# Kernel optimization log

Measured on AMD Instinct MI355X. Metric: run time of the kernel, lower is better.

## Reference

```python
import jax, jax.numpy as jnp
import numpy as np

N, IN_F, OUT_F = 4096, 512, 256
GRAPH_DENSITY = 0.01
NEG_FILL = -1e11  # torch code uses -100000000000.0


def _normalise(g, remove_diagonal):
    # dense branch of normalise_graph (self_connection=False)
    if remove_diagonal:
        g = g - jnp.diag(jnp.diag(g))
    s = g.sum(axis=1)
    s = jnp.where(s == 0.0, 1.0, s)
    d = s ** -0.5
    return d[:, None] * g * d[None, :]


def setup_inputs() -> dict:
    key = jax.random.key(0)
    k1, k2, k3, k4, k5 = jax.random.split(key, 5)
    x = jax.random.normal(k1, (N, IN_F), jnp.float32)
    graph = (jax.random.uniform(k2, (N, N)) < GRAPH_DENSITY).astype(jnp.float32)
    # fc/weight: kaiming-normal-like init
    weight = jax.random.normal(k3, (OUT_F, IN_F), jnp.float32) * np.float32(np.sqrt(2.0 / IN_F))
    t_s = jax.random.normal(k4, (1, OUT_F), jnp.float32) * 0.05
    t_r = jax.random.normal(k5, (1, OUT_F), jnp.float32) * 0.05
    return {"x": x, "graph": graph, "weight": weight, "t_s": t_s, "t_r": t_r}


def reference(x, graph, weight, t_s, t_r):
    # H_ = input @ weight.T   (no bias, no dropout)
    H = x @ weight.T  # [N, OUT_F]

    # get_mask(graph, power=1): normalise(remove_diag) then normalise again
    mask = _normalise(_normalise(graph, remove_diagonal=True), remove_diagonal=False)  # [N, N]

    # get_edge_index_attention, dense path, attention_features == 1
    C1 = jax.nn.leaky_relu(H @ t_s.T, negative_slope=0.2)       # [N, 1]
    C2 = jax.nn.leaky_relu(H @ t_r.T, negative_slope=0.2).T    # [1, N]
    S = (mask * C1 + mask * C2) * 0.5                           # [N, N]
    S = jnp.where(mask <= 0.0, NEG_FILL, S)
    A = jax.nn.softmax(S, axis=1)                               # neighbourhood softmax

    # normalise_graph(A, remove_diagonal=False, self_connection=True), dense path
    A = A + jnp.eye(A.shape[0], dtype=A.dtype)
    s = A.sum(axis=1)
    s = jnp.where(s == 0.0, 1.0, s)
    d = s ** -0.5
    C = d[:, None] * A * d[None, :]

    return C @ H  # [N, OUT_F]
```

## Files before the change

### kernel.cpp

```cpp
#include <hip/hip_runtime.h>
#include <hip/hip_bf16.h>
#include <math.h>

#define N 4096
#define IN_F 512
#define OUT_F 256
#define CAP 128

typedef __attribute__((ext_vector_type(8))) short short8;
typedef __attribute__((ext_vector_type(4))) float float4v;

static __device__ __forceinline__ ushort f2bf(float f) {
  unsigned u = __float_as_uint(f);
  unsigned rnd = 0x7fffu + ((u >> 16) & 1u);
  return (ushort)((u + rnd) >> 16);
}

__global__ __launch_bounds__(256) void build_csr(
    const float* __restrict__ g, int* __restrict__ cols,
    int* __restrict__ deg, float* __restrict__ d1,
    float* __restrict__ c1r, float* __restrict__ c2r) {
  int i = blockIdx.x;
  __shared__ int s_cnt;
  if (threadIdx.x == 0) { s_cnt = 0; c1r[i] = 0.f; c2r[i] = 0.f; }
  __syncthreads();
  const float4* row4 = (const float4*)(g + (size_t)i * N);
  int lane = threadIdx.x & 63;
  for (int it = threadIdx.x; it < N / 4; it += 256) {
    float4 v = row4[it];
    int jb = it * 4;
    bool nz0 = (v.x != 0.f) && (jb + 0 != i);
    bool nz1 = (v.y != 0.f) && (jb + 1 != i);
    bool nz2 = (v.z != 0.f) && (jb + 2 != i);
    bool nz3 = (v.w != 0.f) && (jb + 3 != i);
    unsigned long long m0 = __ballot(nz0);
    unsigned long long m1 = __ballot(nz1);
    unsigned long long m2 = __ballot(nz2);
    unsigned long long m3 = __ballot(nz3);
    int p0 = __popcll(m0), p1 = __popcll(m1), p2 = __popcll(m2), p3 = __popcll(m3);
    int total = p0 + p1 + p2 + p3;
    if (total > 0) {
      int base;
      if (lane == 0) base = atomicAdd(&s_cnt, total);
      base = __shfl(base, 0);
      unsigned long long ltm = (1ull << lane) - 1ull;
      if (nz0) { int p = base + __popcll(m0 & ltm);                 if (p < CAP) cols[(size_t)i * CAP + p] = jb + 0; }
      if (nz1) { int p = base + p0 + __popcll(m1 & ltm);            if (p < CAP) cols[(size_t)i * CAP + p] = jb + 1; }
      if (nz2) { int p = base + p0 + p1 + __popcll(m2 & ltm);       if (p < CAP) cols[(size_t)i * CAP + p] = jb + 2; }
      if (nz3) { int p = base + p0 + p1 + p2 + __popcll(m3 & ltm);  if (p < CAP) cols[(size_t)i * CAP + p] = jb + 3; }
    }
  }
  __syncthreads();
  if (threadIdx.x == 0) {
    int c = s_cnt;
    deg[i] = (c > CAP) ? CAP : c;
    d1[i] = (c == 0) ? 1.f : rsqrtf((float)c);
  }
}

#define LDST 72
__global__ __launch_bounds__(256) void gemm_fused(
    const float* __restrict__ x, const float* __restrict__ wgt,
    const float* __restrict__ ts, const float* __restrict__ tr,
    const int* __restrict__ cols, const int* __restrict__ deg,
    const float* __restrict__ d1, float* __restrict__ w,
    float* __restrict__ H, float* __restrict__ c1r, float* __restrict__ c2r) {
  int bid = blockIdx.x;
  if (bid >= 256) {
    int i = (bid - 256) * 256 + threadIdx.x;
    int dgi = deg[i];
    float sum = 0.f;
    for (int k = 0; k < dgi; ++k) sum += d1[cols[(size_t)i * CAP + k]];
    float s2 = d1[i] * sum;
    float dd2 = (s2 == 0.f) ? 1.f : rsqrtf(s2);
    w[i] = d1[i] * dd2;
    return;
  }
  __shared__ __align__(16) ushort As[64 * LDST];
  __shared__ __align__(16) ushort Bs[64 * LDST];
  int bm = (bid >> 2) * 64;
  int bn = (bid & 3) * 64;
  int tid = threadIdx.x;
  int lane = tid & 63;
  int wv = tid >> 6;
  int wm = (wv >> 1) * 32, wn = (wv & 1) * 32;

  float4v acc[2][2] = {{{0.f,0.f,0.f,0.f},{0.f,0.f,0.f,0.f}},
                       {{0.f,0.f,0.f,0.f},{0.f,0.f,0.f,0.f}}};

  for (int k0 = 0; k0 < IN_F; k0 += 64) {
    #pragma unroll
    for (int p = 0; p < 4; ++p) {
      int idx = p * 256 + tid;
      int row = idx >> 4;
      int cg = idx & 15;
      float4 va = *(const float4*)(x   + (size_t)(bm + row) * IN_F + k0 + cg * 4);
      float4 vb = *(const float4*)(wgt + (size_t)(bn + row) * IN_F + k0 + cg * 4);
      ushort4 pa, pb;
      pa.x = f2bf(va.x); pa.y = f2bf(va.y); pa.z = f2bf(va.z); pa.w = f2bf(va.w);
      pb.x = f2bf(vb.x); pb.y = f2bf(vb.y); pb.z = f2bf(vb.z); pb.w = f2bf(vb.w);
      *(ushort4*)(As + row * LDST + cg * 4) = pa;
      *(ushort4*)(Bs + row * LDST + cg * 4) = pb;
    }
    __syncthreads();
    #pragma unroll
    for (int kk = 0; kk < 64; kk += 32) {
      int kof = kk + (lane >> 4) * 8;
      short8 a0 = *(const short8*)(As + (wm +      (lane & 15)) * LDST + kof);
      short8 a1 = *(const short8*)(As + (wm + 16 + (lane & 15)) * LDST + kof);
      short8 b0 = *(const short8*)(Bs + (wn +      (lane & 15)) * LDST + kof);
      short8 b1 = *(const short8*)(Bs + (wn + 16 + (lane & 15)) * LDST + kof);
      acc[0][0] = __builtin_amdgcn_mfma_f32_16x16x32_bf16(a0, b0, acc[0][0], 0, 0, 0);
      acc[0][1] = __builtin_amdgcn_mfma_f32_16x16x32_bf16(a0, b1, acc[0][1], 0, 0, 0);
      acc[1][0] = __builtin_amdgcn_mfma_f32_16x16x32_bf16(a1, b0, acc[1][0], 0, 0, 0);
      acc[1][1] = __builtin_amdgcn_mfma_f32_16x16x32_bf16(a1, b1, acc[1][1], 0, 0, 0);
    }
    __syncthreads();
  }
  int ccol = lane & 15;
  int crow = (lane >> 4) * 4;
  float ts0 = ts[bn + wn + ccol],      ts1 = ts[bn + wn + 16 + ccol];
  float tr0 = tr[bn + wn + ccol],      tr1 = tr[bn + wn + 16 + ccol];
  #pragma unroll
  for (int rt = 0; rt < 2; ++rt) {
    #pragma unroll
    for (int r = 0; r < 4; ++r) {
      float ps = acc[rt][0][r] * ts0 + acc[rt][1][r] * ts1;
      float pr = acc[rt][0][r] * tr0 + acc[rt][1][r] * tr1;
      #pragma unroll
      for (int off = 1; off < 16; off <<= 1) {
        ps += __shfl_xor(ps, off);
        pr += __shfl_xor(pr, off);
      }
      if (ccol == 0) {
        int row = bm + wm + rt * 16 + crow + r;
        atomicAdd(&c1r[row], ps);
        atomicAdd(&c2r[row], pr);
      }
    }
  }
  #pragma unroll
  for (int rt = 0; rt < 2; ++rt)
    #pragma unroll
    for (int ct = 0; ct < 2; ++ct)
      #pragma unroll
      for (int r = 0; r < 4; ++r) {
        int gr = bm + wm + rt * 16 + crow + r;
        int gc = bn + wn + ct * 16 + ccol;
        H[(size_t)gr * OUT_F + gc] = acc[rt][ct][r];
      }
}

__global__ __launch_bounds__(256) void aggregate(
    const float* __restrict__ H, const int* __restrict__ cols,
    const int* __restrict__ deg, const float* __restrict__ w,
    const float* __restrict__ c1r, const float* __restrict__ c2r,
    float* __restrict__ out) {
  __shared__ int sJ[4][CAP];
  __shared__ float sA[4][CAP];
  int wv = threadIdx.x >> 6;
  int lane = threadIdx.x & 63;
  int i = blockIdx.x * 4 + wv;
  int dgi = deg[i];
  float wi = w[i];
  float c1v = c1r[i];
  float ci = c1v > 0.f ? c1v : 0.2f * c1v;

  float S0 = -1e30f, S1 = -1e30f;
  int j0 = 0, j1 = 0;
  if (lane < dgi) {
    j0 = cols[(size_t)i * CAP + lane];
    float c2v = c2r[j0];
    float cj = c2v > 0.f ? c2v : 0.2f * c2v;
    S0 = 0.5f * wi * w[j0] * (ci + cj);
  }
  if (lane + 64 < dgi) {
    j1 = cols[(size_t)i * CAP + lane + 64];
    float c2v = c2r[j1];
    float cj = c2v > 0.f ? c2v : 0.2f * c2v;
    S1 = 0.5f * wi * w[j1] * (ci + cj);
  }
  float mx = fmaxf(S0, S1);
  #pragma unroll
  for (int off = 32; off > 0; off >>= 1) mx = fmaxf(mx, __shfl_xor(mx, off));
  float e0 = (lane < dgi) ? __expf(S0 - mx) : 0.f;
  float e1 = (lane + 64 < dgi) ? __expf(S1 - mx) : 0.f;
  float Z = e0 + e1;
  #pragma unroll
  for (int off = 32; off > 0; off >>= 1) Z += __shfl_xor(Z, off);
  if (lane < dgi)      { sJ[wv][lane] = j0;        sA[wv][lane] = e0 / Z; }
  if (lane + 64 < dgi) { sJ[wv][lane + 64] = j1;   sA[wv][lane + 64] = e1 / Z; }
  __syncthreads();

  float4 accv = ((const float4*)(H + (size_t)i * OUT_F))[lane];
  if (dgi > 0) {
    int k = 0;
    for (; k + 1 < dgi; k += 2) {
      int ja = sJ[wv][k], jb = sJ[wv][k + 1];
      float aa = sA[wv][k], ab = sA[wv][k + 1];
      float4 ha = ((const float4*)(H + (size_t)ja * OUT_F))[lane];
      float4 hb = ((const float4*)(H + (size_t)jb * OUT_F))[lane];
      accv.x += aa * ha.x + ab * hb.x;
      accv.y += aa * ha.y + ab * hb.y;
      accv.z += aa * ha.z + ab * hb.z;
      accv.w += aa * ha.w + ab * hb.w;
    }
    if (k < dgi) {
      int ja = sJ[wv][k];
      float aa = sA[wv][k];
      float4 ha = ((const float4*)(H + (size_t)ja * OUT_F))[lane];
      accv.x += aa * ha.x; accv.y += aa * ha.y;
      accv.z += aa * ha.z; accv.w += aa * ha.w;
    }
  } else {
    float4 s = {0.f, 0.f, 0.f, 0.f};
    for (int r = 0; r < N; ++r) {
      float4 h = ((const float4*)(H + (size_t)r * OUT_F))[lane];
      s.x += h.x; s.y += h.y; s.z += h.z; s.w += h.w;
    }
    const float inv = 1.f / (float)N;
    accv.x += s.x * inv; accv.y += s.y * inv;
    accv.z += s.z * inv; accv.w += s.w * inv;
  }
  float4 o;
  o.x = 0.5f * accv.x; o.y = 0.5f * accv.y;
  o.z = 0.5f * accv.z; o.w = 0.5f * accv.w;
  ((float4*)(out + (size_t)i * OUT_F))[lane] = o;
}

extern "C" void kernel_launch(void* const* d_in, const int* in_sizes, int n_in,
                              void* d_out, int out_size, void* d_ws, size_t ws_size,
                              hipStream_t stream) {
  const float* x     = (const float*)d_in[0];
  const float* graph = (const float*)d_in[1];
  const float* wgt   = (const float*)d_in[2];
  const float* ts    = (const float*)d_in[3];
  const float* tr    = (const float*)d_in[4];
  float* out = (float*)d_out;

  char* ws = (char*)d_ws;
  float* H    = (float*)(ws);
  int*   cols = (int*)  (ws + (size_t)4 * 1024 * 1024);
  int*   deg  = (int*)  (ws + (size_t)6 * 1024 * 1024);
  float* d1   = (float*)(ws + (size_t)6 * 1024 * 1024 + 16384);
  float* w    = (float*)(ws + (size_t)6 * 1024 * 1024 + 32768);
  float* c1r  = (float*)(ws + (size_t)6 * 1024 * 1024 + 49152);
  float* c2r  = (float*)(ws + (size_t)6 * 1024 * 1024 + 65536);

  build_csr<<<N, 256, 0, stream>>>(graph, cols, deg, d1, c1r, c2r);
  gemm_fused<<<272, 256, 0, stream>>>(x, wgt, ts, tr, cols, deg, d1, w, H, c1r, c2r);
  aggregate<<<N / 4, 256, 0, stream>>>(H, cols, deg, w, c1r, c2r, out);
}
```

Baseline: 137.8 us.

## Co-schedule CSR build with GEMM and move row stats into separate kernel

Merges the CSR-building kernel into the GEMM launch as extra blocks, so the dense graph scan and the bf16 MFMA projection run concurrently instead of back to back. The c1/c2 atomics are removed from the GEMM epilogue. A new rowstats kernel computes the attention projections from H, the degree normalisation, and packed per-row coefficients (ab, uv), which lets aggregate compute each score with two FMAs. The aggregation loop is unrolled by four for more memory-level parallelism. The cost is an extra launch and a re-read of H.

```diff
diff --git a/kernel.cpp b/kernel.cpp
--- a/kernel.cpp
+++ b/kernel.cpp
@@ -1,11 +1,11 @@
 #include <hip/hip_runtime.h>
-#include <hip/hip_bf16.h>
 #include <math.h>
 
 #define N 4096
 #define IN_F 512
 #define OUT_F 256
 #define CAP 128
+#define LDST 72
 
 typedef __attribute__((ext_vector_type(8))) short short8;
 typedef __attribute__((ext_vector_type(4))) float float4v;
@@ -16,72 +16,62 @@
   return (ushort)((u + rnd) >> 16);
 }
 
-__global__ __launch_bounds__(256) void build_csr(
-    const float* __restrict__ g, int* __restrict__ cols,
-    int* __restrict__ deg, float* __restrict__ d1,
-    float* __restrict__ c1r, float* __restrict__ c2r) {
-  int i = blockIdx.x;
-  __shared__ int s_cnt;
-  if (threadIdx.x == 0) { s_cnt = 0; c1r[i] = 0.f; c2r[i] = 0.f; }
-  __syncthreads();
-  const float4* row4 = (const float4*)(g + (size_t)i * N);
-  int lane = threadIdx.x & 63;
-  for (int it = threadIdx.x; it < N / 4; it += 256) {
-    float4 v = row4[it];
-    int jb = it * 4;
-    bool nz0 = (v.x != 0.f) && (jb + 0 != i);
-    bool nz1 = (v.y != 0.f) && (jb + 1 != i);
-    bool nz2 = (v.z != 0.f) && (jb + 2 != i);
-    bool nz3 = (v.w != 0.f) && (jb + 3 != i);
-    unsigned long long m0 = __ballot(nz0);
-    unsigned long long m1 = __ballot(nz1);
-    unsigned long long m2 = __ballot(nz2);
-    unsigned long long m3 = __ballot(nz3);
-    int p0 = __popcll(m0), p1 = __popcll(m1), p2 = __popcll(m2), p3 = __popcll(m3);
-    int total = p0 + p1 + p2 + p3;
-    if (total > 0) {
-      int base;
-      if (lane == 0) base = atomicAdd(&s_cnt, total);
-      base = __shfl(base, 0);
-      unsigned long long ltm = (1ull << lane) - 1ull;
-      if (nz0) { int p = base + __popcll(m0 & ltm);                 if (p < CAP) cols[(size_t)i * CAP + p] = jb + 0; }
-      if (nz1) { int p = base + p0 + __popcll(m1 & ltm);            if (p < CAP) cols[(size_t)i * CAP + p] = jb + 1; }
-      if (nz2) { int p = base + p0 + p1 + __popcll(m2 & ltm);       if (p < CAP) cols[(size_t)i * CAP + p] = jb + 2; }
-      if (nz3) { int p = base + p0 + p1 + p2 + __popcll(m3 & ltm);  if (p < CAP) cols[(size_t)i * CAP + p] = jb + 3; }
-    }
-  }
-  __syncthreads();
-  if (threadIdx.x == 0) {
-    int c = s_cnt;
-    deg[i] = (c > CAP) ? CAP : c;
-    d1[i] = (c == 0) ? 1.f : rsqrtf((float)c);
-  }
-}
-
-#define LDST 72
-__global__ __launch_bounds__(256) void gemm_fused(
-    const float* __restrict__ x, const float* __restrict__ wgt,
-    const float* __restrict__ ts, const float* __restrict__ tr,
-    const int* __restrict__ cols, const int* __restrict__ deg,
-    const float* __restrict__ d1, float* __restrict__ w,
-    float* __restrict__ H, float* __restrict__ c1r, float* __restrict__ c2r) {
-  int bid = blockIdx.x;
-  if (bid >= 256) {
-    int i = (bid - 256) * 256 + threadIdx.x;
-    int dgi = deg[i];
-    float sum = 0.f;
-    for (int k = 0; k < dgi; ++k) sum += d1[cols[(size_t)i * CAP + k]];
-    float s2 = d1[i] * sum;
-    float dd2 = (s2 == 0.f) ? 1.f : rsqrtf(s2);
-    w[i] = d1[i] * dd2;
-    return;
-  }
+static __device__ __forceinline__ float leaky(float v) {
+  return v > 0.f ? v : 0.2f * v;
+}
+
+__global__ __launch_bounds__(256) void csr_gemm(
+    const float* __restrict__ g, const float* __restrict__ x,
+    const float* __restrict__ wgt,
+    int* __restrict__ cols, int* __restrict__ deg, float* __restrict__ d1,
+    float* __restrict__ H) {
   __shared__ __align__(16) ushort As[64 * LDST];
   __shared__ __align__(16) ushort Bs[64 * LDST];
+  __shared__ int s_cnt;
+  int bid = blockIdx.x;
+  int tid = threadIdx.x;
+  int lane = tid & 63;
+
+  if (bid >= 256) {
+    int i = bid - 256;
+    if (tid == 0) s_cnt = 0;
+    __syncthreads();
+    const float4* row4 = (const float4*)(g + (size_t)i * N);
+    for (int it = tid; it < N / 4; it += 256) {
+      float4 v = row4[it];
+      int jb = it * 4;
+      bool nz0 = (v.x != 0.f) && (jb + 0 != i);
+      bool nz1 = (v.y != 0.f) && (jb + 1 != i);
+      bool nz2 = (v.z != 0.f) && (jb + 2 != i);
+      bool nz3 = (v.w != 0.f) && (jb + 3 != i);
+      unsigned long long m0 = __ballot(nz0);
+      unsigned long long m1 = __ballot(nz1);
+      unsigned long long m2 = __ballot(nz2);
+      unsigned long long m3 = __ballot(nz3);
+      int p0 = __popcll(m0), p1 = __popcll(m1), p2 = __popcll(m2), p3 = __popcll(m3);
+      int total = p0 + p1 + p2 + p3;
+      if (total > 0) {
+        int base;
+        if (lane == 0) base = atomicAdd(&s_cnt, total);
+        base = __shfl(base, 0);
+        unsigned long long ltm = (1ull << lane) - 1ull;
+        if (nz0) { int p = base + __popcll(m0 & ltm);                 if (p < CAP) cols[(size_t)i * CAP + p] = jb + 0; }
+        if (nz1) { int p = base + p0 + __popcll(m1 & ltm);            if (p < CAP) cols[(size_t)i * CAP + p] = jb + 1; }
+        if (nz2) { int p = base + p0 + p1 + __popcll(m2 & ltm);       if (p < CAP) cols[(size_t)i * CAP + p] = jb + 2; }
+        if (nz3) { int p = base + p0 + p1 + p2 + __popcll(m3 & ltm);  if (p < CAP) cols[(size_t)i * CAP + p] = jb + 3; }
+      }
+    }
+    __syncthreads();
+    if (tid == 0) {
+      int c = s_cnt;
+      deg[i] = (c > CAP) ? CAP : c;
+      d1[i] = (c == 0) ? 1.f : rsqrtf((float)c);
+    }
+    return;
+  }
+
   int bm = (bid >> 2) * 64;
   int bn = (bid & 3) * 64;
-  int tid = threadIdx.x;
-  int lane = tid & 63;
   int wv = tid >> 6;
   int wm = (wv >> 1) * 32, wn = (wv & 1) * 32;
 
@@ -119,26 +109,6 @@
   }
   int ccol = lane & 15;
   int crow = (lane >> 4) * 4;
-  float ts0 = ts[bn + wn + ccol],      ts1 = ts[bn + wn + 16 + ccol];
-  float tr0 = tr[bn + wn + ccol],      tr1 = tr[bn + wn + 16 + ccol];
-  #pragma unroll
-  for (int rt = 0; rt < 2; ++rt) {
-    #pragma unroll
-    for (int r = 0; r < 4; ++r) {
-      float ps = acc[rt][0][r] * ts0 + acc[rt][1][r] * ts1;
-      float pr = acc[rt][0][r] * tr0 + acc[rt][1][r] * tr1;
-      #pragma unroll
-      for (int off = 1; off < 16; off <<= 1) {
-        ps += __shfl_xor(ps, off);
-        pr += __shfl_xor(pr, off);
-      }
-      if (ccol == 0) {
-        int row = bm + wm + rt * 16 + crow + r;
-        atomicAdd(&c1r[row], ps);
-        atomicAdd(&c2r[row], pr);
-      }
-    }
-  }
   #pragma unroll
   for (int rt = 0; rt < 2; ++rt)
     #pragma unroll
@@ -151,34 +121,68 @@
       }
 }
 
+__global__ __launch_bounds__(256) void rowstats(
+    const int* __restrict__ cols, const int* __restrict__ deg,
+    const float* __restrict__ d1, const float* __restrict__ H,
+    const float* __restrict__ ts, const float* __restrict__ tr,
+    float2* __restrict__ ab, float2* __restrict__ uv) {
+  int wv = threadIdx.x >> 6;
+  int lane = threadIdx.x & 63;
+  int i = blockIdx.x * 4 + wv;
+  int dg = deg[i];
+
+  float s = 0.f;
+  if (lane < dg)       s  = d1[cols[(size_t)i * CAP + lane]];
+  if (lane + 64 < dg)  s += d1[cols[(size_t)i * CAP + lane + 64]];
+
+  float4 h  = ((const float4*)(H + (size_t)i * OUT_F))[lane];
+  float4 t1 = ((const float4*)ts)[lane];
+  float4 t2 = ((const float4*)tr)[lane];
+  float p1 = h.x * t1.x + h.y * t1.y + h.z * t1.z + h.w * t1.w;
+  float p2 = h.x * t2.x + h.y * t2.y + h.z * t2.z + h.w * t2.w;
+
+  #pragma unroll
+  for (int off = 32; off > 0; off >>= 1) {
+    s  += __shfl_xor(s, off);
+    p1 += __shfl_xor(p1, off);
+    p2 += __shfl_xor(p2, off);
+  }
+
+  if (lane == 0) {
+    float di = d1[i];
+    float s2 = di * s;
+    float dd2 = (s2 == 0.f) ? 1.f : rsqrtf(s2);
+    float w = di * dd2;
+    float2 a; a.x = 0.5f * w * leaky(p1); a.y = 0.5f * w;
+    float2 u; u.x = w;                    u.y = w * leaky(p2);
+    ab[i] = a;
+    uv[i] = u;
+  }
+}
+
 __global__ __launch_bounds__(256) void aggregate(
     const float* __restrict__ H, const int* __restrict__ cols,
-    const int* __restrict__ deg, const float* __restrict__ w,
-    const float* __restrict__ c1r, const float* __restrict__ c2r,
-    float* __restrict__ out) {
+    const int* __restrict__ deg, const float2* __restrict__ ab,
+    const float2* __restrict__ uv, float* __restrict__ out) {
   __shared__ int sJ[4][CAP];
   __shared__ float sA[4][CAP];
   int wv = threadIdx.x >> 6;
   int lane = threadIdx.x & 63;
   int i = blockIdx.x * 4 + wv;
   int dgi = deg[i];
-  float wi = w[i];
-  float c1v = c1r[i];
-  float ci = c1v > 0.f ? c1v : 0.2f * c1v;
+  float2 abi = ab[i];
 
   float S0 = -1e30f, S1 = -1e30f;
   int j0 = 0, j1 = 0;
   if (lane < dgi) {
     j0 = cols[(size_t)i * CAP + lane];
-    float c2v = c2r[j0];
-    float cj = c2v > 0.f ? c2v : 0.2f * c2v;
-    S0 = 0.5f * wi * w[j0] * (ci + cj);
+    float2 u = uv[j0];
+    S0 = abi.x * u.x + abi.y * u.y;
   }
   if (lane + 64 < dgi) {
     j1 = cols[(size_t)i * CAP + lane + 64];
-    float c2v = c2r[j1];
-    float cj = c2v > 0.f ? c2v : 0.2f * c2v;
-    S1 = 0.5f * wi * w[j1] * (ci + cj);
+    float2 u = uv[j1];
+    S1 = abi.x * u.x + abi.y * u.y;
   }
   float mx = fmaxf(S0, S1);
   #pragma unroll
@@ -195,17 +199,21 @@
   float4 accv = ((const float4*)(H + (size_t)i * OUT_F))[lane];
   if (dgi > 0) {
     int k = 0;
-    for (; k + 1 < dgi; k += 2) {
-      int ja = sJ[wv][k], jb = sJ[wv][k + 1];
-      float aa = sA[wv][k], ab = sA[wv][k + 1];
+    for (; k + 3 < dgi; k += 4) {
+      int ja = sJ[wv][k],     jb = sJ[wv][k + 1];
+      int jc = sJ[wv][k + 2], jd = sJ[wv][k + 3];
+      float aa = sA[wv][k],     abw = sA[wv][k + 1];
+      float ac = sA[wv][k + 2], ad  = sA[wv][k + 3];
       float4 ha = ((const float4*)(H + (size_t)ja * OUT_F))[lane];
       float4 hb = ((const float4*)(H + (size_t)jb * OUT_F))[lane];
-      accv.x += aa * ha.x + ab * hb.x;
-      accv.y += aa * ha.y + ab * hb.y;
-      accv.z += aa * ha.z + ab * hb.z;
-      accv.w += aa * ha.w + ab * hb.w;
-    }
-    if (k < dgi) {
+      float4 hc = ((const float4*)(H + (size_t)jc * OUT_F))[lane];
+      float4 hd = ((const float4*)(H + (size_t)jd * OUT_F))[lane];
+      accv.x += aa * ha.x + abw * hb.x + ac * hc.x + ad * hd.x;
+      accv.y += aa * ha.y + abw * hb.y + ac * hc.y + ad * hd.y;
+      accv.z += aa * ha.z + abw * hb.z + ac * hc.z + ad * hd.z;
+      accv.w += aa * ha.w + abw * hb.w + ac * hc.w + ad * hd.w;
+    }
+    for (; k < dgi; ++k) {
       int ja = sJ[wv][k];
       float aa = sA[wv][k];
       float4 ha = ((const float4*)(H + (size_t)ja * OUT_F))[lane];
@@ -239,15 +247,14 @@
   float* out = (float*)d_out;
 
   char* ws = (char*)d_ws;
-  float* H    = (float*)(ws);
-  int*   cols = (int*)  (ws + (size_t)4 * 1024 * 1024);
-  int*   deg  = (int*)  (ws + (size_t)6 * 1024 * 1024);
-  float* d1   = (float*)(ws + (size_t)6 * 1024 * 1024 + 16384);
-  float* w    = (float*)(ws + (size_t)6 * 1024 * 1024 + 32768);
-  float* c1r  = (float*)(ws + (size_t)6 * 1024 * 1024 + 49152);
-  float* c2r  = (float*)(ws + (size_t)6 * 1024 * 1024 + 65536);
-
-  build_csr<<<N, 256, 0, stream>>>(graph, cols, deg, d1, c1r, c2r);
-  gemm_fused<<<272, 256, 0, stream>>>(x, wgt, ts, tr, cols, deg, d1, w, H, c1r, c2r);
-  aggregate<<<N / 4, 256, 0, stream>>>(H, cols, deg, w, c1r, c2r, out);
-}
+  float*  H    = (float*) (ws);
+  int*    cols = (int*)   (ws + (size_t)4 * 1024 * 1024);
+  int*    deg  = (int*)   (ws + (size_t)6 * 1024 * 1024);
+  float*  d1   = (float*) (ws + (size_t)6 * 1024 * 1024 + 16384);
+  float2* ab   = (float2*)(ws + (size_t)6 * 1024 * 1024 + 32768);
+  float2* uv   = (float2*)(ws + (size_t)6 * 1024 * 1024 + 65536);
+
+  csr_gemm<<<4096 + 256, 256, 0, stream>>>(graph, x, wgt, cols, deg, d1, H);
+  rowstats<<<N / 4, 256, 0, stream>>>(cols, deg, d1, H, ts, tr, ab, uv);
+  aggregate<<<N / 4, 256, 0, stream>>>(H, cols, deg, ab, uv, out);
+}
```

Result: faster. 134.9 us (-2.1%).
